# Kernel tuning notes

Hardware: AMD Instinct MI355X
Metric: run time of the kernel (lower is better)

Reference implementation:

```python
import jax, jax.numpy as jnp
import numpy as np

B, T, C, K = 8, 2048, 1024, 128

def setup_inputs() -> dict:
    key = jax.random.key(0)
    k1, k2, k3, k4 = jax.random.split(key, 4)
    scale = 0.02
    return {
        "x": jax.random.normal(k1, (B, T, C), dtype=jnp.float32),
        "Wq": jax.random.normal(k2, (C, K), dtype=jnp.float32) * scale,
        "Wk": jax.random.normal(k3, (C, K), dtype=jnp.float32) * scale,
        "Wv": jax.random.normal(k4, (C, K), dtype=jnp.float32) * scale,
    }

def reference(x, Wq, Wk, Wv):
    # Single-head causal self-attention (ModulUwagi.forward)
    q = jnp.einsum('btc,ck->btk', x, Wq)  # [B,T,K]
    k = jnp.einsum('btc,ck->btk', x, Wk)
    v = jnp.einsum('btc,ck->btk', x, Wv)
    hd = q.shape[-1]
    wei = jnp.einsum('btk,bsk->bts', q, k) * (hd ** -0.5)  # [B,T,T]
    causal = jnp.tril(jnp.ones((x.shape[1], x.shape[1]), dtype=bool))
    wei = jnp.where(causal, wei, -jnp.inf)
    wei = jax.nn.softmax(wei, axis=-1)
    out = jnp.einsum('bts,bsk->btk', wei, v)  # [B,T,K]
    return out
```

## Files before the change

### kernel.cpp

```cpp
#include <hip/hip_runtime.h>
#include <cmath>

#define Bn 8
#define Tn 2048
#define Cn 1024
#define Kn 128

typedef __attribute__((ext_vector_type(8))) short short8;
typedef __attribute__((ext_vector_type(4))) float f32x4;
typedef unsigned short u16;
typedef unsigned int u32;

#define NEGINF (-__builtin_huge_valf())

__device__ __forceinline__ u16 f2b(float f) {
    u32 u = __float_as_uint(f);
    u32 r = (u + 0x7FFFu + ((u >> 16) & 1u)) >> 16;
    return (u16)r;
}
__device__ __forceinline__ float b2f(u16 v) {
    u32 u = ((u32)v) << 16;
    return __uint_as_float(u);
}
__device__ __forceinline__ u32 cvtpk(float lo, float hi) {
    u32 r;
    asm("v_cvt_pk_bf16_f32 %0, %1, %2" : "=v"(r) : "v"(lo), "v"(hi));
    return r;
}

__device__ __forceinline__ void load_lds16(const u16* g, u16* l) {
    __builtin_amdgcn_global_load_lds(
        (const __attribute__((address_space(1))) u32*)(g),
        (__attribute__((address_space(3))) u32*)(l), 16, 0, 0);
}

__global__ __launch_bounds__(256)
void prep_kernel(const float* __restrict__ Wq, const float* __restrict__ Wk,
                 const float* __restrict__ Wv, u16* __restrict__ Wt)
{
    int id = blockIdx.x * 256 + threadIdx.x;
    int w   = id >> 15;
    int rem = id & 32767;
    int c   = rem >> 5;
    int n4  = (rem & 31) << 2;
    const float* W = (w == 0) ? Wq : (w == 1) ? Wk : Wv;
    float4 v = *(const float4*)(W + (size_t)c * Kn + n4);
    u16* dst = Wt + (size_t)w * Kn * Cn;
    dst[(size_t)(n4 + 0) * Cn + c] = f2b(v.x);
    dst[(size_t)(n4 + 1) * Cn + c] = f2b(v.y);
    dst[(size_t)(n4 + 2) * Cn + c] = f2b(v.z);
    dst[(size_t)(n4 + 3) * Cn + c] = f2b(v.w);
}

__global__ __launch_bounds__(256)
void proj5_kernel(const float* __restrict__ x, const u16* __restrict__ Wt,
                  u16* __restrict__ qkv)
{
    const int bid = blockIdx.x;
    const int g8  = bid >> 3, xr = bid & 7;
    const int w   = g8 % 3;
    const int rt  = (g8 / 3) * 8 + xr;
    const u16* wtg = Wt + (size_t)w * Kn * Cn;
    u16* outp = qkv + (size_t)w * Bn * Tn * Kn;
    const int row0 = rt * 64;
    const int tid  = threadIdx.x;
    const int lane = tid & 63;
    const int wid  = tid >> 6;
    const int l15  = lane & 15, lh = lane >> 4;
    const int m0 = (wid >> 1) * 32, n0 = (wid & 1) * 64;

    __shared__ u16 lds[24576];

    auto stageW = [&](int kk, int buf) {
        #pragma unroll
        for (int i = 0; i < 4; ++i) {
            int u = tid + i * 256;
            int n = u >> 3, c8 = u & 7;
            load_lds16(wtg + (size_t)n * Cn + kk + ((c8 ^ (n & 7)) << 3),
                       lds + 8192 + buf * 8192 + u * 8);
        }
    };
    auto loadX = [&](int kk, float4* xr4) {
        #pragma unroll
        for (int i = 0; i < 2; ++i) {
            int u = tid + i * 256;
            int r = u >> 3, c8 = u & 7;
            const float* s = x + (size_t)(row0 + r) * Cn + kk + c8 * 8;
            xr4[2 * i]     = *(const float4*)(s);
            xr4[2 * i + 1] = *(const float4*)(s + 4);
        }
    };
    auto writeX = [&](int buf, const float4* xr4) {
        u16* dst = lds + buf * 4096;
        #pragma unroll
        for (int i = 0; i < 2; ++i) {
            int u = tid + i * 256;
            int r = u >> 3, c8 = u & 7;
            uint4 pk;
            pk.x = cvtpk(xr4[2 * i].x,     xr4[2 * i].y);
            pk.y = cvtpk(xr4[2 * i].z,     xr4[2 * i].w);
            pk.z = cvtpk(xr4[2 * i + 1].x, xr4[2 * i + 1].y);
            pk.w = cvtpk(xr4[2 * i + 1].z, xr4[2 * i + 1].w);
            *(uint4*)(dst + r * 64 + ((c8 ^ (r & 7)) << 3)) = pk;
        }
    };

    f32x4 acc[2][4];
    #pragma unroll
    for (int i = 0; i < 2; ++i)
        #pragma unroll
        for (int j = 0; j < 4; ++j) acc[i][j] = (f32x4){0.f, 0.f, 0.f, 0.f};

    auto compute = [&](int buf) {
        const u16* Xb = lds + buf * 4096;
        const u16* Wb = lds + 8192 + buf * 8192;
        #pragma unroll
        for (int kc = 0; kc < 2; ++kc) {
            short8 af[2], bf[4];
            #pragma unroll
            for (int mg = 0; mg < 2; ++mg) {
                int row = m0 + mg * 16 + l15;
                int ch  = (kc * 4 + lh) ^ (row & 7);
                af[mg] = *(const short8*)(Xb + row * 64 + ch * 8);
            }
            #pragma unroll
            for (int ng = 0; ng < 4; ++ng) {
                int n  = n0 + ng * 16 + l15;
                int ch = (kc * 4 + lh) ^ (n & 7);
                bf[ng] = *(const short8*)(Wb + n * 64 + ch * 8);
            }
            #pragma unroll
            for (int mg = 0; mg < 2; ++mg)
                #pragma unroll
                for (int ng = 0; ng < 4; ++ng)
                    acc[mg][ng] = __builtin_amdgcn_mfma_f32_16x16x32_bf16(
                        af[mg], bf[ng], acc[mg][ng], 0, 0, 0);
        }
    };

    float4 xA[4], xB[4];
    loadX(0, xA);
    stageW(0, 0);
    loadX(64, xB);
    writeX(0, xA);
    asm volatile("s_waitcnt vmcnt(4) lgkmcnt(0)" ::: "memory");
    __builtin_amdgcn_sched_barrier(0);
    __builtin_amdgcn_s_barrier();
    __builtin_amdgcn_sched_barrier(0);

    auto step = [&](int t, float4* XW, float4* XL) {
        const int buf = t & 1;
        if (t + 1 < 16) stageW((t + 1) * 64, buf ^ 1);
        if (t + 2 < 16) loadX((t + 2) * 64, XL);
        compute(buf);
        if (t + 1 < 16) writeX(buf ^ 1, XW);
        if (t < 15) {
            if (t < 14)
                asm volatile("s_waitcnt vmcnt(4) lgkmcnt(0)" ::: "memory");
            else
                asm volatile("s_waitcnt vmcnt(0) lgkmcnt(0)" ::: "memory");
            __builtin_amdgcn_sched_barrier(0);
            __builtin_amdgcn_s_barrier();
            __builtin_amdgcn_sched_barrier(0);
        }
    };

    for (int tt = 0; tt < 8; ++tt) {
        step(2 * tt,     xB, xA);
        step(2 * tt + 1, xA, xB);
    }

    #pragma unroll
    for (int mg = 0; mg < 2; ++mg)
        #pragma unroll
        for (int ng = 0; ng < 4; ++ng)
            #pragma unroll
            for (int r = 0; r < 4; ++r) {
                int m = row0 + m0 + mg * 16 + lh * 4 + r;
                int n = n0 + ng * 16 + l15;
                outp[(size_t)m * Kn + n] = f2b(acc[mg][ng][r]);
            }
}

__device__ const int g_job_qi[32] = {0, 1,1, 2,2,2, 3,3,3,3, 4,4,4,4,
                                     5,5,5,5,5, 6,6,6,6,6,6, 7,7,7,7,7,7,7};
__device__ const int g_sup_b[32] = {0, 0,4, 0,4,8, 0,4,8,12, 0,5,10,15,
                                    0,4,9,14,19, 0,4,9,14,18,23, 0,4,9,13,18,22,27};
__device__ const int g_sup_e[32] = {4, 4,8, 4,8,12, 4,8,12,16, 5,10,15,20,
                                    4,9,14,19,24, 4,9,14,18,23,28, 4,9,13,18,22,27,32};

__global__ __launch_bounds__(512, 2)
void attn_kernel(const u16* __restrict__ qg_, const u16* __restrict__ kg_,
                 const u16* __restrict__ vg_, u16* __restrict__ pO,
                 float* __restrict__ pM, float* __restrict__ pL)
{
    const int b   = blockIdx.x;
    const int job = blockIdx.y;
    const int qi  = g_job_qi[job];
    const int sb  = g_sup_b[job], se = g_sup_e[job];

    const u16* qw = qg_ + (size_t)b * Tn * Kn;
    const u16* kw = kg_ + (size_t)b * Tn * Kn;
    const u16* vw = vg_ + (size_t)b * Tn * Kn;

    const int tid  = threadIdx.x;
    const int lane = tid & 63;
    const int wid  = tid >> 6;
    const int l15  = lane & 15, lh = lane >> 4;

    const int q0 = qi * 256 + wid * 32;
    const int qmax_w = q0 + 31;

    __shared__ u16 lds[32768];

    short8 qf[2][4];
    #pragma unroll
    for (int g = 0; g < 2; ++g)
        #pragma unroll
        for (int kc = 0; kc < 4; ++kc)
            qf[g][kc] = *(const short8*)(qw + (size_t)(q0 + g * 16 + l15) * Kn
                                         + kc * 32 + lh * 8);

    f32x4 acc[8][2];
    #pragma unroll
    for (int dt = 0; dt < 8; ++dt)
        #pragma unroll
        for (int g = 0; g < 2; ++g) acc[dt][g] = (f32x4){0.f, 0.f, 0.f, 0.f};
    float m_g[2] = {NEGINF, NEGINF}, l_g[2] = {0.f, 0.f};

    const float scale = 0.08838834764831843f;

    auto stageK = [&](int sup, int buf) {
        const u16* src = kw + (size_t)sup * 64 * Kn;
        u16* dst = lds + buf * 8192;
        #pragma unroll
        for (int i = 0; i < 2; ++i) {
            int u = wid * 128 + i * 64 + lane;
            int row = u >> 4;
            int c16 = (u & 15) ^ (row & 7);
            load_lds16(src + (size_t)row * Kn + c16 * 8,
                       dst + (size_t)(wid * 128 + i * 64) * 8);
        }
    };
    auto loadV = [&](int sup, uint4* vr) {
        const u16* src = vw + (size_t)sup * 64 * Kn;
        #pragma unroll
        for (int r = 0; r < 2; ++r) {
            int s  = tid & 63;
            int u8 = (tid >> 6) + 8 * r;
            vr[r] = *(const uint4*)(src + (size_t)s * Kn + u8 * 8);
        }
    };
    auto writeV = [&](int buf, const uint4* vr) {
        u16* dst = lds + 16384 + buf * 8192;
        #pragma unroll
        for (int r = 0; r < 2; ++r) {
            int s  = tid & 63;
            int u8 = (tid >> 6) + 8 * r;
            const u16* e = (const u16*)&vr[r];
            #pragma unroll
            for (int j = 0; j < 8; ++j) {
                int d = u8 * 8 + j;
                dst[d * 64 + (((s >> 3) ^ j) << 3) + (s & 7)] = e[j];
            }
        }
    };

    uint4 vreg[2];
    stageK(sb, 0);
    loadV(sb, vreg);
    writeV(0, vreg);

    for (int sup = sb; sup < se; ++sup) {
        const int cur = (sup - sb) & 1;
        __syncthreads();
        const bool have_next = (sup + 1 < se);
        if (have_next) {
            stageK(sup + 1, cur ^ 1);
            loadV(sup + 1, vreg);
        }
        if (sup * 64 <= qmax_w) {
            const u16* Kb = lds + cur * 8192;
            const u16* Vb = lds + 16384 + cur * 8192;
            f32x4 sf[4][2];
            #pragma unroll
            for (int mt = 0; mt < 4; ++mt)
                #pragma unroll
                for (int g = 0; g < 2; ++g) sf[mt][g] = (f32x4){0.f,0.f,0.f,0.f};
            #pragma unroll
            for (int kc = 0; kc < 4; ++kc) {
                short8 a[4];
                #pragma unroll
                for (int mt = 0; mt < 4; ++mt) {
                    int row = mt * 16 + l15;
                    int ch  = (kc * 4 + lh) ^ (row & 7);
                    a[mt] = *(const short8*)(Kb + row * 128 + ch * 8);
                }
                #pragma unroll
                for (int mt = 0; mt < 4; ++mt)
                    #pragma unroll
                    for (int g = 0; g < 2; ++g)
                        sf[mt][g] = __builtin_amdgcn_mfma_f32_16x16x32_bf16(
                            a[mt], qf[g][kc], sf[mt][g], 0, 0, 0);
            }
            const int sbase = sup * 64;

            float pvv[2][16];
            float pmax2[2];
            #pragma unroll
            for (int g = 0; g < 2; ++g) {
                const int qg = q0 + g * 16 + l15;
                float pm = NEGINF;
                #pragma unroll
                for (int mt = 0; mt < 4; ++mt)
                    #pragma unroll
                    for (int r = 0; r < 4; ++r) {
                        int sg = sbase + mt * 16 + lh * 4 + r;
                        float vv = sf[mt][g][r] * scale;
                        vv = (sg > qg) ? NEGINF : vv;
                        pvv[g][mt * 4 + r] = vv;
                        pm = fmaxf(pm, vv);
                    }
                pm = fmaxf(pm, __shfl_xor(pm, 16));
                pm = fmaxf(pm, __shfl_xor(pm, 32));
                pmax2[g] = pm;
            }

            const bool defer = __all((pmax2[0] - m_g[0] <= 8.f) &&
                                     (pmax2[1] - m_g[1] <= 8.f));

            u32 upk[2][4][2];
            float alpha_g[2];
            #pragma unroll
            for (int g = 0; g < 2; ++g) {
                float mns;
                if (defer) {
                    mns = m_g[g];
                    alpha_g[g] = 1.f;
                } else {
                    float mn = fmaxf(m_g[g], pmax2[g]);
                    mns = (mn == NEGINF) ? 0.f : mn;
                    alpha_g[g] = __expf(m_g[g] - mns);
                    m_g[g] = mn;
                }
                float ps = 0.f;
                #pragma unroll
                for (int i = 0; i < 16; ++i) {
                    pvv[g][i] = __expf(pvv[g][i] - mns);
                    ps += pvv[g][i];
                }
                ps += __shfl_xor(ps, 16);
                ps += __shfl_xor(ps, 32);
                l_g[g] = l_g[g] * alpha_g[g] + ps;
                #pragma unroll
                for (int mt = 0; mt < 4; ++mt)
                    #pragma unroll
                    for (int h = 0; h < 2; ++h)
                        upk[g][mt][h] = (u32)f2b(pvv[g][mt * 4 + 2 * h])
                                      | ((u32)f2b(pvv[g][mt * 4 + 2 * h + 1]) << 16);
            }
            if (!defer) {
                #pragma unroll
                for (int dt = 0; dt < 8; ++dt)
                    #pragma unroll
                    for (int g = 0; g < 2; ++g)
                        acc[dt][g] *= alpha_g[g];
            }
            #pragma unroll
            for (int ks = 0; ks < 2; ++ks) {
                short8 pf[2];
                #pragma unroll
                for (int g = 0; g < 2; ++g) {
                    union { u32 w[4]; short8 v; } uu;
                    #pragma unroll
                    for (int hp = 0; hp < 4; ++hp) {
                        int srcLane = l15 + 16 * ((lh & 1) * 2 + (hp >> 1));
                        u32 vA = __shfl(upk[g][2 * ks][hp & 1], srcLane, 64);
                        u32 vB = __shfl(upk[g][2 * ks + 1][hp & 1], srcLane, 64);
                        uu.w[hp] = (lh < 2) ? vA : vB;
                    }
                    pf[g] = uu.v;
                }
                #pragma unroll
                for (int dt = 0; dt < 8; ++dt) {
                    int d  = dt * 16 + l15;
                    int ch = (ks * 4 + lh) ^ (d & 7);
                    short8 av = *(const short8*)(Vb + d * 64 + ch * 8);
                    #pragma unroll
                    for (int g = 0; g < 2; ++g)
                        acc[dt][g] = __builtin_amdgcn_mfma_f32_16x16x32_bf16(
                            av, pf[g], acc[dt][g], 0, 0, 0);
                }
            }
        }
        if (have_next) writeV(cur ^ 1, vreg);
    }

    const size_t slotrow = ((size_t)b * 32 + job) * 256 + wid * 32;
    #pragma unroll
    for (int g = 0; g < 2; ++g) {
        size_t row = slotrow + g * 16 + l15;
        #pragma unroll
        for (int dt = 0; dt < 8; ++dt) {
            ushort4 o = { f2b(acc[dt][g][0]), f2b(acc[dt][g][1]),
                          f2b(acc[dt][g][2]), f2b(acc[dt][g][3]) };
            *(ushort4*)(pO + row * 128 + dt * 16 + lh * 4) = o;
        }
        if (lh == 0) {
            pM[row] = m_g[g];
            pL[row] = l_g[g];
        }
    }
}

__device__ const int g_cnt[8] = {1, 2, 3, 4, 4, 5, 6, 7};
__device__ const int g_s0[8]  = {0, 1, 3, 6, 10, 14, 19, 25};

__global__ __launch_bounds__(256)
void merge_kernel(const u16* __restrict__ pO, const float* __restrict__ pM,
                  const float* __restrict__ pL, float* __restrict__ out)
{
    const int bid = blockIdx.x;
    const int b   = bid >> 8;
    const int rem = bid & 255;
    const int qi  = rem >> 5;
    const int rg  = rem & 31;
    const int c = g_cnt[qi], s0 = g_s0[qi];
    const int tid = threadIdx.x;
    const int r8 = tid >> 5;
    const int dg = tid & 31;

    const int row = rg * 8 + r8;
    const size_t base = ((size_t)b * 32 + s0) * 256 + row;

    float mv[8];
    float M = NEGINF;
    #pragma unroll
    for (int i = 0; i < 8; ++i)
        if (i < c) { mv[i] = pM[base + (size_t)i * 256]; M = fmaxf(M, mv[i]); }
    float L = 0.f, w[8];
    #pragma unroll
    for (int i = 0; i < 8; ++i)
        if (i < c) {
            float e = __expf(mv[i] - M);
            L += pL[base + (size_t)i * 256] * e;
            w[i] = e;
        }
    const float invL = 1.f / L;

    float4 o = {0.f, 0.f, 0.f, 0.f};
    #pragma unroll
    for (int i = 0; i < 8; ++i)
        if (i < c) {
            ushort4 p = *(const ushort4*)(pO + (base + (size_t)i * 256) * 128 + dg * 4);
            float wi = w[i] * invL;
            o.x = fmaf(wi, b2f(p.x), o.x);
            o.y = fmaf(wi, b2f(p.y), o.y);
            o.z = fmaf(wi, b2f(p.z), o.z);
            o.w = fmaf(wi, b2f(p.w), o.w);
        }
    *(float4*)(out + ((size_t)b * Tn + qi * 256 + row) * Kn + dg * 4) = o;
}

extern "C" void kernel_launch(void* const* d_in, const int* in_sizes, int n_in,
                              void* d_out, int out_size, void* d_ws, size_t ws_size,
                              hipStream_t stream)
{
    const float* x  = (const float*)d_in[0];
    const float* Wq = (const float*)d_in[1];
    const float* Wk = (const float*)d_in[2];
    const float* Wv = (const float*)d_in[3];
    float* out = (float*)d_out;

    u16* ws = (u16*)d_ws;
    const size_t btk = (size_t)Bn * Tn * Kn;
    u16* q  = ws;
    u16* k  = ws + btk;
    u16* v  = ws + 2 * btk;
    u16* Wt = ws + 3 * btk;
    u16* pO = ws + 3 * btk + 393216;
    float* pM = (float*)(pO + (size_t)8388608);
    float* pL = pM + 65536;

    prep_kernel<<<384, 256, 0, stream>>>(Wq, Wk, Wv, Wt);
    proj5_kernel<<<768, 256, 0, stream>>>(x, Wt, ws);
    attn_kernel<<<dim3(Bn, 32), 512, 0, stream>>>(q, k, v, pO, pM, pL);
    merge_kernel<<<2048, 256, 0, stream>>>(pO, pM, pL, out);
}
```

Measured before the change: 67.65 us.

## Deepen projection kernel pipeline to triple-buffered W and X prefetch

Changes the QKV projection GEMM so the W tile is triple-buffered in LDS and the X tile is held in three register sets instead of two. Loads run two or three k-steps ahead, and the vmcnt waits are relaxed to match the deeper queue. The aim is to hide more global-memory latency behind MFMA compute. The cost is more LDS (64KB per block) and more registers, which may lower occupancy.

```diff
diff --git a/kernel.cpp b/kernel.cpp
--- a/kernel.cpp
+++ b/kernel.cpp
@@ -53,7 +53,7 @@
 }
 
 __global__ __launch_bounds__(256)
-void proj5_kernel(const float* __restrict__ x, const u16* __restrict__ Wt,
+void proj7_kernel(const float* __restrict__ x, const u16* __restrict__ Wt,
                   u16* __restrict__ qkv)
 {
     const int bid = blockIdx.x;
@@ -69,7 +69,7 @@
     const int l15  = lane & 15, lh = lane >> 4;
     const int m0 = (wid >> 1) * 32, n0 = (wid & 1) * 64;
 
-    __shared__ u16 lds[24576];
+    __shared__ u16 lds[32768];
 
     auto stageW = [&](int kk, int buf) {
         #pragma unroll
@@ -111,9 +111,9 @@
         #pragma unroll
         for (int j = 0; j < 4; ++j) acc[i][j] = (f32x4){0.f, 0.f, 0.f, 0.f};
 
-    auto compute = [&](int buf) {
-        const u16* Xb = lds + buf * 4096;
-        const u16* Wb = lds + 8192 + buf * 8192;
+    auto compute = [&](int xb, int wb) {
+        const u16* Xb = lds + xb * 4096;
+        const u16* Wb = lds + 8192 + wb * 8192;
         #pragma unroll
         for (int kc = 0; kc < 2; ++kc) {
             short8 af[2], bf[4];
@@ -138,25 +138,30 @@
         }
     };
 
-    float4 xA[4], xB[4];
+    float4 xA[4], xB[4], xC[4];
+    stageW(0, 0);
     loadX(0, xA);
-    stageW(0, 0);
+    stageW(64, 1);
     loadX(64, xB);
+    loadX(128, xC);
     writeX(0, xA);
-    asm volatile("s_waitcnt vmcnt(4) lgkmcnt(0)" ::: "memory");
+    asm volatile("s_waitcnt lgkmcnt(0)" ::: "memory");
     __builtin_amdgcn_sched_barrier(0);
     __builtin_amdgcn_s_barrier();
     __builtin_amdgcn_sched_barrier(0);
 
-    auto step = [&](int t, float4* XW, float4* XL) {
-        const int buf = t & 1;
-        if (t + 1 < 16) stageW((t + 1) * 64, buf ^ 1);
-        if (t + 2 < 16) loadX((t + 2) * 64, XL);
-        compute(buf);
-        if (t + 1 < 16) writeX(buf ^ 1, XW);
+    auto step = [&](int t, float4* xW, float4* xL) {
+        const int xb = t & 1;
+        const int wb = t % 3;
+        if (t + 2 < 16) stageW((t + 2) * 64, (t + 2) % 3);
+        if (t + 3 < 16) loadX((t + 3) * 64, xL);
+        compute(xb, wb);
+        if (t + 1 < 16) writeX(xb ^ 1, xW);
         if (t < 15) {
-            if (t < 14)
-                asm volatile("s_waitcnt vmcnt(4) lgkmcnt(0)" ::: "memory");
+            if (t <= 12)
+                asm volatile("s_waitcnt vmcnt(12) lgkmcnt(0)" ::: "memory");
+            else if (t == 13)
+                asm volatile("s_waitcnt vmcnt(8) lgkmcnt(0)" ::: "memory");
             else
                 asm volatile("s_waitcnt vmcnt(0) lgkmcnt(0)" ::: "memory");
             __builtin_amdgcn_sched_barrier(0);
@@ -165,10 +170,12 @@
         }
     };
 
-    for (int tt = 0; tt < 8; ++tt) {
-        step(2 * tt,     xB, xA);
-        step(2 * tt + 1, xA, xB);
+    for (int tt = 0; tt < 5; ++tt) {
+        step(3 * tt,     xB, xA);
+        step(3 * tt + 1, xC, xB);
+        step(3 * tt + 2, xA, xC);
     }
+    step(15, xB, xA);
 
     #pragma unroll
     for (int mg = 0; mg < 2; ++mg)
@@ -483,7 +490,7 @@
     float* pL = pM + 65536;
 
     prep_kernel<<<384, 256, 0, stream>>>(Wq, Wk, Wv, Wt);
-    proj5_kernel<<<768, 256, 0, stream>>>(x, Wt, ws);
+    proj7_kernel<<<768, 256, 0, stream>>>(x, Wt, ws);
     attn_kernel<<<dim3(Bn, 32), 512, 0, stream>>>(q, k, v, pO, pM, pL);
     merge_kernel<<<2048, 256, 0, stream>>>(pO, pM, pL, out);
 }
```

Result: slower. 74.97 us (+10.8%).

## Fuse split-KV merge into attention kernel via last-block atomic counter

Applied to the files above, without the earlier changes.

Removes the separate merge kernel launch. Each attention block atomically increments a per-(batch, query-tile) counter after writing its partial output, and the last block to finish for that tile performs the softmax-weighted merge and writes the final output. This trades one kernel launch and its tail for a threadfence, an atomic, and a serialized merge done by a single 512-thread block per tile, plus a memset of the counters each call.

```diff
diff --git a/kernel.cpp b/kernel.cpp
--- a/kernel.cpp
+++ b/kernel.cpp
@@ -188,11 +188,14 @@
                                     0,4,9,14,19, 0,4,9,14,18,23, 0,4,9,13,18,22,27};
 __device__ const int g_sup_e[32] = {4, 4,8, 4,8,12, 4,8,12,16, 5,10,15,20,
                                     4,9,14,19,24, 4,9,14,18,23,28, 4,9,13,18,22,27,32};
+__device__ const int g_cnt[8] = {1, 2, 3, 4, 4, 5, 6, 7};
+__device__ const int g_s0[8]  = {0, 1, 3, 6, 10, 14, 19, 25};
 
 __global__ __launch_bounds__(512, 2)
 void attn_kernel(const u16* __restrict__ qg_, const u16* __restrict__ kg_,
                  const u16* __restrict__ vg_, u16* __restrict__ pO,
-                 float* __restrict__ pM, float* __restrict__ pL)
+                 float* __restrict__ pM, float* __restrict__ pL,
+                 int* __restrict__ cnts, float* __restrict__ out)
 {
     const int b   = blockIdx.x;
     const int job = blockIdx.y;
@@ -411,55 +414,50 @@
             pL[row] = l_g[g];
         }
     }
-}
-
-__device__ const int g_cnt[8] = {1, 2, 3, 4, 4, 5, 6, 7};
-__device__ const int g_s0[8]  = {0, 1, 3, 6, 10, 14, 19, 25};
-
-__global__ __launch_bounds__(256)
-void merge_kernel(const u16* __restrict__ pO, const float* __restrict__ pM,
-                  const float* __restrict__ pL, float* __restrict__ out)
-{
-    const int bid = blockIdx.x;
-    const int b   = bid >> 8;
-    const int rem = bid & 255;
-    const int qi  = rem >> 5;
-    const int rg  = rem & 31;
-    const int c = g_cnt[qi], s0 = g_s0[qi];
-    const int tid = threadIdx.x;
-    const int r8 = tid >> 5;
-    const int dg = tid & 31;
-
-    const int row = rg * 8 + r8;
-    const size_t base = ((size_t)b * 32 + s0) * 256 + row;
-
-    float mv[8];
-    float M = NEGINF;
-    #pragma unroll
-    for (int i = 0; i < 8; ++i)
-        if (i < c) { mv[i] = pM[base + (size_t)i * 256]; M = fmaxf(M, mv[i]); }
-    float L = 0.f, w[8];
-    #pragma unroll
-    for (int i = 0; i < 8; ++i)
-        if (i < c) {
-            float e = __expf(mv[i] - M);
-            L += pL[base + (size_t)i * 256] * e;
-            w[i] = e;
-        }
-    const float invL = 1.f / L;
-
-    float4 o = {0.f, 0.f, 0.f, 0.f};
-    #pragma unroll
-    for (int i = 0; i < 8; ++i)
-        if (i < c) {
-            ushort4 p = *(const ushort4*)(pO + (base + (size_t)i * 256) * 128 + dg * 4);
-            float wi = w[i] * invL;
-            o.x = fmaf(wi, b2f(p.x), o.x);
-            o.y = fmaf(wi, b2f(p.y), o.y);
-            o.z = fmaf(wi, b2f(p.z), o.z);
-            o.w = fmaf(wi, b2f(p.w), o.w);
-        }
-    *(float4*)(out + ((size_t)b * Tn + qi * 256 + row) * Kn + dg * 4) = o;
+
+    __threadfence();
+    __syncthreads();
+    volatile int* flag = (volatile int*)lds;
+    if (tid == 0) {
+        int old = atomicAdd(&cnts[b * 8 + qi], 1);
+        *flag = (old + 1 == g_cnt[qi]) ? 1 : 0;
+    }
+    __syncthreads();
+    if (*flag) {
+        __threadfence();
+        const int c  = g_cnt[qi], s0 = g_s0[qi];
+        const int r16 = tid >> 5;
+        const int dg  = tid & 31;
+        for (int rr = r16; rr < 256; rr += 16) {
+            const size_t base = ((size_t)b * 32 + s0) * 256 + rr;
+            float mv[8];
+            float M = NEGINF;
+            #pragma unroll
+            for (int i = 0; i < 8; ++i)
+                if (i < c) { mv[i] = pM[base + (size_t)i * 256]; M = fmaxf(M, mv[i]); }
+            float L = 0.f, wgt[8];
+            #pragma unroll
+            for (int i = 0; i < 8; ++i)
+                if (i < c) {
+                    float e = __expf(mv[i] - M);
+                    L += pL[base + (size_t)i * 256] * e;
+                    wgt[i] = e;
+                }
+            const float invL = 1.f / L;
+            float4 o = {0.f, 0.f, 0.f, 0.f};
+            #pragma unroll
+            for (int i = 0; i < 8; ++i)
+                if (i < c) {
+                    ushort4 p = *(const ushort4*)(pO + (base + (size_t)i * 256) * 128 + dg * 4);
+                    float wi = wgt[i] * invL;
+                    o.x = fmaf(wi, b2f(p.x), o.x);
+                    o.y = fmaf(wi, b2f(p.y), o.y);
+                    o.z = fmaf(wi, b2f(p.z), o.z);
+                    o.w = fmaf(wi, b2f(p.w), o.w);
+                }
+            *(float4*)(out + ((size_t)b * Tn + qi * 256 + rr) * Kn + dg * 4) = o;
+        }
+    }
 }
 
 extern "C" void kernel_launch(void* const* d_in, const int* in_sizes, int n_in,
@@ -481,9 +479,10 @@
     u16* pO = ws + 3 * btk + 393216;
     float* pM = (float*)(pO + (size_t)8388608);
     float* pL = pM + 65536;
-
+    int*   cnt = (int*)(pL + 65536);
+
+    hipMemsetAsync(cnt, 0, 64 * sizeof(int), stream);
     prep_kernel<<<384, 256, 0, stream>>>(Wq, Wk, Wv, Wt);
     proj5_kernel<<<768, 256, 0, stream>>>(x, Wt, ws);
-    attn_kernel<<<dim3(Bn, 32), 512, 0, stream>>>(q, k, v, pO, pM, pL);
-    merge_kernel<<<2048, 256, 0, stream>>>(pO, pM, pL, out);
-}
+    attn_kernel<<<dim3(Bn, 32), 512, 0, stream>>>(q, k, v, pO, pM, pL, cnt, out);
+}
```

Result: slower. 209.6 us (+209.9%).
